# Kernel tuning notes

Measured on AMD Instinct MI355X. Metric: run time of the kernel, lower is better.

Reference implementation:

```python
import jax, jax.numpy as jnp
import numpy as np

EPS = 1e-5

def _conv1x1(x, w, b):
    # x: (B,C,H,W), w: (O,C), b: (O,)
    return jnp.einsum('oc,bchw->bohw', w, x) + b[None, :, None, None]

def setup_inputs() -> dict:
    key = jax.random.key(0)
    ks = jax.random.split(key, 11)
    B, C, H, W = 8, 256, 48, 48
    return {
        'x': jax.random.normal(ks[0], (B, C, H, W), jnp.float32),
        'g_w': jax.random.normal(ks[1], (1, C), jnp.float32) * 0.05,
        'g_b': jax.random.normal(ks[2], (1,), jnp.float32) * 0.05,
        'theta_w': jax.random.normal(ks[3], (1, C), jnp.float32) * 0.05,
        'theta_b': jax.random.normal(ks[4], (1,), jnp.float32) * 0.05,
        'phi_w': jax.random.normal(ks[5], (1, C), jnp.float32) * 0.05,
        'phi_b': jax.random.normal(ks[6], (1,), jnp.float32) * 0.05,
        'w_w': jax.random.normal(ks[7], (C, 1), jnp.float32) * 0.05,
        'w_b': jax.random.normal(ks[8], (C,), jnp.float32) * 0.05,
        'bn_gamma': jax.random.normal(ks[9], (C,), jnp.float32) * 0.05,
        'bn_beta': jax.random.normal(ks[10], (C,), jnp.float32) * 0.05,
    }

def reference(x, g_w, g_b, theta_w, theta_b, phi_w, phi_b, w_w, w_b, bn_gamma, bn_beta):
    B, C, H, W = x.shape
    N = H * W
    # 1x1 conv projections to inter_channels == 1, flattened over space
    g_x = _conv1x1(x, g_w, g_b).reshape(B, 1, N).transpose(0, 2, 1)        # (B, N, 1)
    theta_x = _conv1x1(x, theta_w, theta_b).reshape(B, 1, N).transpose(0, 2, 1)  # (B, N, 1)
    phi_x = _conv1x1(x, phi_w, phi_b).reshape(B, 1, N)                      # (B, 1, N)
    # non-local attention (softmax-free, constant-N normalization)
    f = jnp.matmul(theta_x, phi_x) / N                                     # (B, N, N)
    y = jnp.matmul(f, g_x)                                                  # (B, N, 1)
    y = y.transpose(0, 2, 1).reshape(B, 1, H, W)
    # W block: conv1x1 (1 -> C) + BatchNorm2d (training-mode batch stats)
    w_y = _conv1x1(y, w_w, w_b)                                             # (B, C, H, W)
    mean = jnp.mean(w_y, axis=(0, 2, 3), keepdims=True)
    var = jnp.mean((w_y - mean) ** 2, axis=(0, 2, 3), keepdims=True)
    w_y = (w_y - mean) * jax.lax.rsqrt(var + EPS)
    w_y = w_y * bn_gamma[None, :, None, None] + bn_beta[None, :, None, None]
    return w_y + x
```

## Files before the change

kernel.cpp:

```cpp
#include <hip/hip_runtime.h>

#define N_SP 2304
#define C_CH 256
#define B_B  8
#define TILES 36
#define BN_EPS 1e-5f

#define WS_THETA 0
#define WS_PG    18432
#define WS_TH    (18432 + 288)
#define WS_TH2   (18432 + 576)

__global__ __launch_bounds__(512) void proj_kernel(
    const float* __restrict__ x,
    const float* __restrict__ gw, const float* __restrict__ gb,
    const float* __restrict__ tw, const float* __restrict__ tb,
    const float* __restrict__ pw, const float* __restrict__ pb,
    float* __restrict__ ws)
{
    __shared__ float pt[8][64], pp[8][64], pgv[8][64];

    const int tid  = threadIdx.x;
    const int w    = tid >> 6;
    const int lane = tid & 63;
    const int blk  = blockIdx.x;
    const int b    = blk / TILES;
    const int tile = blk - b * TILES;

    const int n = tile * 64 + lane;
    const int cbase = __builtin_amdgcn_readfirstlane(w * 32);
    const float* xp = x + (size_t)b * C_CH * N_SP + (size_t)cbase * N_SP + n;

    float at = 0.f, ap = 0.f, ag = 0.f;
    #pragma unroll
    for (int c = 0; c < 32; ++c) {
        float v = xp[(size_t)c * N_SP];
        at = fmaf(tw[cbase + c], v, at);
        ap = fmaf(pw[cbase + c], v, ap);
        ag = fmaf(gw[cbase + c], v, ag);
    }
    pt[w][lane]  = at;
    pp[w][lane]  = ap;
    pgv[w][lane] = ag;
    __syncthreads();

    if (tid < 64) {
        float st = 0.f, sp = 0.f, sg = 0.f;
        #pragma unroll
        for (int j = 0; j < 8; ++j) {
            st += pt[j][tid];
            sp += pp[j][tid];
            sg += pgv[j][tid];
        }
        const float th = st + tb[0];
        const float ph = sp + pb[0];
        const float gg = sg + gb[0];

        ws[WS_THETA + b * N_SP + tile * 64 + tid] = th;

        float r_pg  = ph * gg;
        float r_th  = th;
        float r_th2 = th * th;
        #pragma unroll
        for (int off = 32; off >= 1; off >>= 1) {
            r_pg  += __shfl_xor(r_pg,  off, 64);
            r_th  += __shfl_xor(r_th,  off, 64);
            r_th2 += __shfl_xor(r_th2, off, 64);
        }
        if (tid == 0) {
            ws[WS_PG  + blk] = r_pg;
            ws[WS_TH  + blk] = r_th;
            ws[WS_TH2 + blk] = r_th2;
        }
    }
}

__global__ __launch_bounds__(192) void out_kernel(
    const float* __restrict__ x,  const float* __restrict__ ww,
    const float* __restrict__ gamma, const float* __restrict__ beta,
    const float* __restrict__ ws, float* __restrict__ out)
{
    __shared__ float fS[B_B], fTH[B_B], fTH2[B_B];
    const int tid = threadIdx.x;

    if (tid < 64) {
        const int fb = tid >> 3;
        const int l  = tid & 7;
        float pg = 0.f, th = 0.f, th2 = 0.f;
        #pragma unroll
        for (int k = 0; k < 5; ++k) {
            const int t = l + 8 * k;
            if (t < TILES) {
                pg  += ws[WS_PG  + fb * TILES + t];
                th  += ws[WS_TH  + fb * TILES + t];
                th2 += ws[WS_TH2 + fb * TILES + t];
            }
        }
        #pragma unroll
        for (int off = 4; off >= 1; off >>= 1) {
            pg  += __shfl_xor(pg,  off, 64);
            th  += __shfl_xor(th,  off, 64);
            th2 += __shfl_xor(th2, off, 64);
        }
        if (l == 0) {
            fS[fb]   = pg / (float)N_SP;
            fTH[fb]  = th;
            fTH2[fb] = th2;
        }
    }
    __syncthreads();

    const int bc = blockIdx.x;
    const int b  = bc >> 8;
    const int c  = bc & 255;

    float ybar = 0.f, ey2 = 0.f;
    #pragma unroll
    for (int bb = 0; bb < B_B; ++bb) {
        ybar += fS[bb] * fTH[bb];
        ey2  += fS[bb] * fS[bb] * fTH2[bb];
    }
    const float inv = 1.0f / (float)(B_B * N_SP);
    ybar *= inv;
    ey2  *= inv;
    const float vary = ey2 - ybar * ybar;

    const float wv = ww[c];
    const float sc = gamma[c] * wv * rsqrtf(wv * wv * vary + BN_EPS);
    const float s  = fS[b];
    const float be = beta[c];
    const float yb = ybar;

    const float4* xr   = (const float4*)(x  + (size_t)bc * N_SP);
    const float4* tr   = (const float4*)(ws + WS_THETA + b * N_SP);
    float4*       orow = (float4*)((float*)out + (size_t)bc * N_SP);

    #pragma unroll
    for (int k = 0; k < 3; ++k) {
        const int i = tid + k * 192;
        float4 xv = xr[i];
        float4 tv = tr[i];
        float4 o;
        o.x = fmaf(sc, fmaf(tv.x, s, -yb), xv.x + be);
        o.y = fmaf(sc, fmaf(tv.y, s, -yb), xv.y + be);
        o.z = fmaf(sc, fmaf(tv.z, s, -yb), xv.z + be);
        o.w = fmaf(sc, fmaf(tv.w, s, -yb), xv.w + be);
        orow[i] = o;
    }
}

extern "C" void kernel_launch(void* const* d_in, const int* in_sizes, int n_in,
                              void* d_out, int out_size, void* d_ws, size_t ws_size,
                              hipStream_t stream) {
    const float* x        = (const float*)d_in[0];
    const float* g_w      = (const float*)d_in[1];
    const float* g_b      = (const float*)d_in[2];
    const float* theta_w  = (const float*)d_in[3];
    const float* theta_b  = (const float*)d_in[4];
    const float* phi_w    = (const float*)d_in[5];
    const float* phi_b    = (const float*)d_in[6];
    const float* w_w      = (const float*)d_in[7];
    const float* bn_gamma = (const float*)d_in[9];
    const float* bn_beta  = (const float*)d_in[10];

    float* ws  = (float*)d_ws;
    float* out = (float*)d_out;

    proj_kernel<<<B_B * TILES, 512, 0, stream>>>(x, g_w, g_b, theta_w, theta_b,
                                                 phi_w, phi_b, ws);
    out_kernel<<<B_B * C_CH, 192, 0, stream>>>(x, w_w, bn_gamma, bn_beta, ws, out);
}
```

Baseline: 17.12 us.

## Fuse projection and output kernels with grid-wide atomic barrier and register-held x

Merges the two kernels into one persistent-style kernel. Each block keeps its 32 channels of x in registers, publishes per-tile partial sums, and the last block per batch reduces them. All blocks then spin on a global counter before writing the normalized output directly, which avoids re-reading x and the theta buffer from memory. This relies on all 288 blocks being co-resident, which is why launch_bounds requests 4 blocks per SM, and it adds a memset launch plus spin-wait overhead. The output stores are now strided scalar writes instead of float4 rows.

```diff
diff --git a/kernel.cpp b/kernel.cpp
--- a/kernel.cpp
+++ b/kernel.cpp
@@ -4,21 +4,35 @@
 #define C_CH 256
 #define B_B  8
 #define TILES 36
+#define NBLK (B_B * TILES)
 #define BN_EPS 1e-5f
 
-#define WS_THETA 0
-#define WS_PG    18432
-#define WS_TH    (18432 + 288)
-#define WS_TH2   (18432 + 576)
+#define WS_PG    0
+#define WS_TH    288
+#define WS_TH2   576
+#define WS_BSUM  864
+#define WS_CNT_BYTE 3584
+#define CNT_TOP  128
+#define CNT_MEMSET_BYTES 576
 
-__global__ __launch_bounds__(512) void proj_kernel(
+#define AGENT __HIP_MEMORY_SCOPE_AGENT
+#define RLX   __ATOMIC_RELAXED
+#define ACQ   __ATOMIC_ACQUIRE
+#define AR    __ATOMIC_ACQ_REL
+
+__global__ __launch_bounds__(512, 4) void fused_kernel(
     const float* __restrict__ x,
     const float* __restrict__ gw, const float* __restrict__ gb,
     const float* __restrict__ tw, const float* __restrict__ tb,
     const float* __restrict__ pw, const float* __restrict__ pb,
-    float* __restrict__ ws)
+    const float* __restrict__ ww, const float* __restrict__ gamma,
+    const float* __restrict__ beta,
+    float* __restrict__ ws, int* __restrict__ cnt, float* __restrict__ out)
 {
     __shared__ float pt[8][64], pp[8][64], pgv[8][64];
+    __shared__ float th_lds[64];
+    __shared__ float sB[24];
+    __shared__ int lastFlag;
 
     const int tid  = threadIdx.x;
     const int w    = tid >> 6;
@@ -31,13 +45,14 @@
     const int cbase = __builtin_amdgcn_readfirstlane(w * 32);
     const float* xp = x + (size_t)b * C_CH * N_SP + (size_t)cbase * N_SP + n;
 
+    float xr[32];
     float at = 0.f, ap = 0.f, ag = 0.f;
     #pragma unroll
     for (int c = 0; c < 32; ++c) {
-        float v = xp[(size_t)c * N_SP];
-        at = fmaf(tw[cbase + c], v, at);
-        ap = fmaf(pw[cbase + c], v, ap);
-        ag = fmaf(gw[cbase + c], v, ag);
+        xr[c] = xp[(size_t)c * N_SP];
+        at = fmaf(tw[cbase + c], xr[c], at);
+        ap = fmaf(pw[cbase + c], xr[c], ap);
+        ag = fmaf(gw[cbase + c], xr[c], ag);
     }
     pt[w][lane]  = at;
     pp[w][lane]  = ap;
@@ -56,7 +71,7 @@
         const float ph = sp + pb[0];
         const float gg = sg + gb[0];
 
-        ws[WS_THETA + b * N_SP + tile * 64 + tid] = th;
+        th_lds[tid] = th;
 
         float r_pg  = ph * gg;
         float r_th  = th;
@@ -68,84 +83,70 @@
             r_th2 += __shfl_xor(r_th2, off, 64);
         }
         if (tid == 0) {
-            ws[WS_PG  + blk] = r_pg;
-            ws[WS_TH  + blk] = r_th;
-            ws[WS_TH2 + blk] = r_th2;
+            __hip_atomic_store(&ws[WS_PG  + blk], r_pg,  RLX, AGENT);
+            __hip_atomic_store(&ws[WS_TH  + blk], r_th,  RLX, AGENT);
+            __hip_atomic_store(&ws[WS_TH2 + blk], r_th2, RLX, AGENT);
+            int old = __hip_atomic_fetch_add(&cnt[b * 16], 1, AR, AGENT);
+            lastFlag = (old == TILES - 1);
         }
     }
-}
+    __syncthreads();
 
-__global__ __launch_bounds__(192) void out_kernel(
-    const float* __restrict__ x,  const float* __restrict__ ww,
-    const float* __restrict__ gamma, const float* __restrict__ beta,
-    const float* __restrict__ ws, float* __restrict__ out)
-{
-    __shared__ float fS[B_B], fTH[B_B], fTH2[B_B];
-    const int tid = threadIdx.x;
-
-    if (tid < 64) {
-        const int fb = tid >> 3;
-        const int l  = tid & 7;
+    if (lastFlag && tid < 64) {
         float pg = 0.f, th = 0.f, th2 = 0.f;
-        #pragma unroll
-        for (int k = 0; k < 5; ++k) {
-            const int t = l + 8 * k;
-            if (t < TILES) {
-                pg  += ws[WS_PG  + fb * TILES + t];
-                th  += ws[WS_TH  + fb * TILES + t];
-                th2 += ws[WS_TH2 + fb * TILES + t];
-            }
+        if (tid < TILES) {
+            pg  = __hip_atomic_load(&ws[WS_PG  + b * TILES + tid], RLX, AGENT);
+            th  = __hip_atomic_load(&ws[WS_TH  + b * TILES + tid], RLX, AGENT);
+            th2 = __hip_atomic_load(&ws[WS_TH2 + b * TILES + tid], RLX, AGENT);
         }
         #pragma unroll
-        for (int off = 4; off >= 1; off >>= 1) {
+        for (int off = 32; off >= 1; off >>= 1) {
             pg  += __shfl_xor(pg,  off, 64);
             th  += __shfl_xor(th,  off, 64);
             th2 += __shfl_xor(th2, off, 64);
         }
-        if (l == 0) {
-            fS[fb]   = pg / (float)N_SP;
-            fTH[fb]  = th;
-            fTH2[fb] = th2;
+        if (tid == 0) {
+            __hip_atomic_store(&ws[WS_BSUM + b * 4 + 0], pg,  RLX, AGENT);
+            __hip_atomic_store(&ws[WS_BSUM + b * 4 + 1], th,  RLX, AGENT);
+            __hip_atomic_store(&ws[WS_BSUM + b * 4 + 2], th2, RLX, AGENT);
+            __hip_atomic_fetch_add(&cnt[CNT_TOP], 1, AR, AGENT);
         }
+    }
+
+    if (tid == 0) {
+        while (__hip_atomic_load(&cnt[CNT_TOP], ACQ, AGENT) < B_B)
+            __builtin_amdgcn_s_sleep(1);
     }
     __syncthreads();
 
-    const int bc = blockIdx.x;
-    const int b  = bc >> 8;
-    const int c  = bc & 255;
+    if (tid < 24) {
+        const int bb = tid / 3, k = tid - bb * 3;
+        sB[tid] = __hip_atomic_load(&ws[WS_BSUM + bb * 4 + k], RLX, AGENT);
+    }
+    __syncthreads();
 
     float ybar = 0.f, ey2 = 0.f;
+    const float invN = 1.0f / (float)N_SP;
     #pragma unroll
     for (int bb = 0; bb < B_B; ++bb) {
-        ybar += fS[bb] * fTH[bb];
-        ey2  += fS[bb] * fS[bb] * fTH2[bb];
+        const float sbb = sB[bb * 3 + 0] * invN;
+        ybar += sbb * sB[bb * 3 + 1];
+        ey2  += sbb * sbb * sB[bb * 3 + 2];
     }
     const float inv = 1.0f / (float)(B_B * N_SP);
     ybar *= inv;
     ey2  *= inv;
     const float vary = ey2 - ybar * ybar;
 
-    const float wv = ww[c];
-    const float sc = gamma[c] * wv * rsqrtf(wv * wv * vary + BN_EPS);
-    const float s  = fS[b];
-    const float be = beta[c];
-    const float yb = ybar;
+    const float s   = sB[b * 3 + 0] * invN;
+    const float tsy = fmaf(th_lds[lane], s, -ybar);
 
-    const float4* xr   = (const float4*)(x  + (size_t)bc * N_SP);
-    const float4* tr   = (const float4*)(ws + WS_THETA + b * N_SP);
-    float4*       orow = (float4*)((float*)out + (size_t)bc * N_SP);
-
+    float* op = out + (size_t)b * C_CH * N_SP + (size_t)cbase * N_SP + n;
     #pragma unroll
-    for (int k = 0; k < 3; ++k) {
-        const int i = tid + k * 192;
-        float4 xv = xr[i];
-        float4 tv = tr[i];
-        float4 o;
-        o.x = fmaf(sc, fmaf(tv.x, s, -yb), xv.x + be);
-        o.y = fmaf(sc, fmaf(tv.y, s, -yb), xv.y + be);
-        o.z = fmaf(sc, fmaf(tv.z, s, -yb), xv.z + be);
-        o.w = fmaf(sc, fmaf(tv.w, s, -yb), xv.w + be);
-        orow[i] = o;
+    for (int c = 0; c < 32; ++c) {
+        const float wv = ww[cbase + c];
+        const float sc = gamma[cbase + c] * wv * rsqrtf(fmaf(wv * wv, vary, BN_EPS));
+        op[(size_t)c * N_SP] = fmaf(sc, tsy, xr[c] + beta[cbase + c]);
     }
 }
 
@@ -164,9 +165,11 @@
     const float* bn_beta  = (const float*)d_in[10];
 
     float* ws  = (float*)d_ws;
+    int*   cnt = (int*)((char*)d_ws + WS_CNT_BYTE);
     float* out = (float*)d_out;
 
-    proj_kernel<<<B_B * TILES, 512, 0, stream>>>(x, g_w, g_b, theta_w, theta_b,
-                                                 phi_w, phi_b, ws);
-    out_kernel<<<B_B * C_CH, 192, 0, stream>>>(x, w_w, bn_gamma, bn_beta, ws, out);
+    hipMemsetAsync(cnt, 0, CNT_MEMSET_BYTES, stream);
+    fused_kernel<<<NBLK, 512, 0, stream>>>(x, g_w, g_b, theta_w, theta_b,
+                                           phi_w, phi_b, w_w, bn_gamma, bn_beta,
+                                           ws, cnt, out);
 }
```

Result: slower. 38.02 us (+122.1%).
